# Optimization experiments

Hardware: AMD Instinct MI355X
Metric: run time of the kernel (lower is better)

The kernel has to match this reference:

```python
import jax, jax.numpy as jnp
import numpy as np

D_MODEL = 1024
NUM_HEADS = 16
D_K = D_MODEL // NUM_HEADS


def setup_inputs() -> dict:
    key = jax.random.key(0)
    ks = jax.random.split(key, 5)
    sd = np.sqrt(2.0 / (D_MODEL + D_MODEL))
    x = jax.random.normal(ks[0], (2, 2048, D_MODEL), dtype=jnp.float32)
    # weights stored as [out_features, in_features] like torch Linear
    w_q = jax.random.normal(ks[1], (D_MODEL, D_MODEL), dtype=jnp.float32) * (sd * sd)
    w_k = jax.random.normal(ks[2], (D_MODEL, D_MODEL), dtype=jnp.float32) * (sd * sd)
    w_v = jax.random.normal(ks[3], (D_MODEL, D_MODEL), dtype=jnp.float32) * (sd * sd)
    w_o = jax.random.normal(ks[4], (D_MODEL, D_MODEL), dtype=jnp.float32) * (sd * sd)
    return {"x": x, "w_q": w_q, "w_k": w_k, "w_v": w_v, "w_o": w_o}


def reference(x, w_q, w_k, w_v, w_o):
    B, S, D = x.shape
    H, Dk = NUM_HEADS, D_K
    # projections: x @ W.T
    q = (x @ w_q.T).reshape(B, S, H, Dk).transpose(0, 2, 1, 3)  # [B,H,S,Dk]
    k = (x @ w_k.T).reshape(B, S, H, Dk).transpose(0, 2, 1, 3)
    v = (x @ w_v.T).reshape(B, S, H, Dk).transpose(0, 2, 1, 3)
    scale = 1.0 / np.sqrt(Dk).astype(np.float32)
    scores = jnp.einsum('bhqd,bhkd->bhqk', q, k) * scale  # [B,H,S,S]
    causal = jnp.tril(jnp.ones((S, S), dtype=bool))
    scores = jnp.where(causal, scores, -jnp.inf)
    weights = jax.nn.softmax(scores, axis=-1)
    attn = jnp.einsum('bhqk,bhkd->bhqd', weights, v)  # [B,H,S,Dk]
    attn = attn.transpose(0, 2, 1, 3).reshape(B, S, D)
    return attn @ w_o.T
```

## Files before the change

### kernel.cpp

```cpp
#include <hip/hip_runtime.h>

typedef __attribute__((ext_vector_type(8))) short short8;
typedef __attribute__((ext_vector_type(4))) float f32x4;
typedef __attribute__((ext_vector_type(16))) float f32x16;
typedef __attribute__((ext_vector_type(2))) unsigned int u32x2;

#define DM 1024
#define SL 2048
#define NH 16
#define DKH 64
#define NB 2

__device__ __forceinline__ unsigned short f2bf(float f) {
    union { float f; unsigned int u; } a; a.f = f;
    unsigned int r = a.u + 0x7FFFu + ((a.u >> 16) & 1u);
    return (unsigned short)(r >> 16);
}

__device__ __forceinline__ void gl_lds16(const void* g, void* l) {
    __builtin_amdgcn_global_load_lds(
        (__attribute__((address_space(1))) void*)(g),
        (__attribute__((address_space(3))) void*)(l), 16, 0, 0);
}

__device__ __forceinline__ unsigned int cvtpk_bf16(float lo, float hi) {
    unsigned int r;
    asm("v_cvt_pk_bf16_f32 %0, %1, %2" : "=v"(r) : "v"(lo), "v"(hi));
    return r;
}

__device__ __forceinline__ void pl32swap(unsigned int &a, unsigned int &b) {
    u32x2 r = __builtin_amdgcn_permlane32_swap(a, b, false, false);
    a = r[0]; b = r[1];
}
__device__ __forceinline__ void pl32swapf(float &a, float &b) {
    unsigned int ua = __float_as_uint(a), ub = __float_as_uint(b);
    pl32swap(ua, ub);
    a = __uint_as_float(ua); b = __uint_as_float(ub);
}

__global__ __launch_bounds__(256) void convert_kernel(
    const float* __restrict__ x,  const float* __restrict__ wq,
    const float* __restrict__ wk, const float* __restrict__ wv,
    const float* __restrict__ wo,
    unsigned short* __restrict__ xb,  unsigned short* __restrict__ wqb,
    unsigned short* __restrict__ wkb, unsigned short* __restrict__ wvb,
    unsigned short* __restrict__ wob)
{
    const int NX = NB * SL * DM;
    const int NW = DM * DM;
    int t4 = (blockIdx.x * 256 + threadIdx.x) * 4;
    const float* src; unsigned short* dst; int off; float scale = 1.0f;
    if (t4 < NX)              { src = x;  dst = xb;  off = t4; }
    else if (t4 < NX + NW)    { src = wq; dst = wqb; off = t4 - NX; scale = 0.125f * 1.44269504088896f; }
    else if (t4 < NX + 2*NW)  { src = wk; dst = wkb; off = t4 - NX - NW; }
    else if (t4 < NX + 3*NW)  { src = wv; dst = wvb; off = t4 - NX - 2*NW; }
    else                      { src = wo; dst = wob; off = t4 - NX - 3*NW; }
    float4 v = *(const float4*)(src + off);
    unsigned long long p =
        (unsigned long long)f2bf(v.x * scale)
      | ((unsigned long long)f2bf(v.y * scale) << 16)
      | ((unsigned long long)f2bf(v.z * scale) << 32)
      | ((unsigned long long)f2bf(v.w * scale) << 48);
    *(unsigned long long*)(dst + off) = p;
}

__global__ __launch_bounds__(256) void gemm_bt(
    const unsigned short* __restrict__ A,
    const unsigned short* __restrict__ Bw,
    unsigned short* __restrict__ oq, unsigned short* __restrict__ ok,
    unsigned short* __restrict__ ov)
{
    __shared__ __align__(16) unsigned short As[128 * 64];
    __shared__ __align__(16) unsigned short Bs[128 * 64];
    const int tid  = threadIdx.x;
    const int lane = tid & 63;
    const int wave = tid >> 6;
    const int wm = (wave >> 1) * 64, wn = (wave & 1) * 64;
    const int bx = blockIdx.x, by = blockIdx.y;
    const int c    = lane & 15;
    const int kg16 = (lane >> 4) * 16;
    const int swz  = (c & 7) << 4;

    f32x4 acc[4][4];
    #pragma unroll
    for (int i = 0; i < 4; i++)
        #pragma unroll
        for (int j = 0; j < 4; j++) acc[i][j] = (f32x4){0.f, 0.f, 0.f, 0.f};

    const char* Ab = (const char*)A  + by * 128 * (DM * 2);
    const char* Bb = (const char*)Bw + bx * 128 * (DM * 2);

    for (int k0 = 0; k0 < DM; k0 += 64) {
        #pragma unroll
        for (int i = 0; i < 4; i++) {
            int o  = i * 4096 + tid * 16;
            int r  = o >> 7;
            int cb = o & 127;
            int src = r * (DM * 2) + k0 * 2 + (cb ^ ((r & 7) << 4));
            gl_lds16(Ab + src, (char*)As + o);
            gl_lds16(Bb + src, (char*)Bs + o);
        }
        __syncthreads();
        #pragma unroll
        for (int kk = 0; kk < 2; kk++) {
            short8 a[4], bfr[4];
            #pragma unroll
            for (int mi = 0; mi < 4; mi++)
                a[mi] = *(const short8*)((const char*)As
                        + (wm + mi * 16 + c) * 128 + ((kk * 64 + kg16) ^ swz));
            #pragma unroll
            for (int ni = 0; ni < 4; ni++)
                bfr[ni] = *(const short8*)((const char*)Bs
                        + (wn + ni * 16 + c) * 128 + ((kk * 64 + kg16) ^ swz));
            #pragma unroll
            for (int mi = 0; mi < 4; mi++)
                #pragma unroll
                for (int ni = 0; ni < 4; ni++)
                    acc[mi][ni] = __builtin_amdgcn_mfma_f32_16x16x32_bf16(
                        a[mi], bfr[ni], acc[mi][ni], 0, 0, 0);
        }
        __syncthreads();
    }

    const int r4 = (lane >> 4) * 4;
    const int mat = (bx * 128) >> 10;
    unsigned short* outb = (mat == 0) ? oq : (mat == 1) ? ok : ov;
    const int nb = bx * 128 - (mat << 10);
    #pragma unroll
    for (int mi = 0; mi < 4; mi++) {
        int m_g = by * 128 + wm + mi * 16 + r4;
        int b_  = m_g >> 11, s_ = m_g & 2047;
        #pragma unroll
        for (int ni = 0; ni < 4; ni++) {
            int n_l = nb + wn + ni * 16 + c;
            int h = n_l >> 6, dk = n_l & 63;
            #pragma unroll
            for (int j = 0; j < 4; j++)
                outb[((b_ * NH + h) * SL + (s_ + j)) * DKH + dk] = f2bf(acc[mi][ni][j]);
        }
    }
}

__global__ __launch_bounds__(256) void gemm_o(
    const unsigned short* __restrict__ A,
    const unsigned short* __restrict__ Bw,
    float* __restrict__ of)
{
    __shared__ __align__(16) unsigned short As[64 * 64];
    __shared__ __align__(16) unsigned short Bs[128 * 64];
    const int tid  = threadIdx.x;
    const int lane = tid & 63;
    const int wave = tid >> 6;
    const int wm = (wave >> 1) * 32, wn = (wave & 1) * 64;
    const int bx = blockIdx.x, by = blockIdx.y;
    const int c    = lane & 15;
    const int kg16 = (lane >> 4) * 16;
    const int swz  = (c & 7) << 4;

    f32x4 acc[2][4];
    #pragma unroll
    for (int i = 0; i < 2; i++)
        #pragma unroll
        for (int j = 0; j < 4; j++) acc[i][j] = (f32x4){0.f, 0.f, 0.f, 0.f};

    const char* Ab = (const char*)A  + by * 64  * (DM * 2);
    const char* Bb = (const char*)Bw + bx * 128 * (DM * 2);

    for (int k0 = 0; k0 < DM; k0 += 64) {
        #pragma unroll
        for (int i = 0; i < 2; i++) {
            int o  = i * 4096 + tid * 16;
            int r  = o >> 7, cb = o & 127;
            int src = r * (DM * 2) + k0 * 2 + (cb ^ ((r & 7) << 4));
            gl_lds16(Ab + src, (char*)As + o);
        }
        #pragma unroll
        for (int i = 0; i < 4; i++) {
            int o  = i * 4096 + tid * 16;
            int r  = o >> 7, cb = o & 127;
            int src = r * (DM * 2) + k0 * 2 + (cb ^ ((r & 7) << 4));
            gl_lds16(Bb + src, (char*)Bs + o);
        }
        __syncthreads();
        #pragma unroll
        for (int kk = 0; kk < 2; kk++) {
            short8 a[2], bfr[4];
            #pragma unroll
            for (int mi = 0; mi < 2; mi++)
                a[mi] = *(const short8*)((const char*)As
                        + (wm + mi * 16 + c) * 128 + ((kk * 64 + kg16) ^ swz));
            #pragma unroll
            for (int ni = 0; ni < 4; ni++)
                bfr[ni] = *(const short8*)((const char*)Bs
                        + (wn + ni * 16 + c) * 128 + ((kk * 64 + kg16) ^ swz));
            #pragma unroll
            for (int mi = 0; mi < 2; mi++)
                #pragma unroll
                for (int ni = 0; ni < 4; ni++)
                    acc[mi][ni] = __builtin_amdgcn_mfma_f32_16x16x32_bf16(
                        a[mi], bfr[ni], acc[mi][ni], 0, 0, 0);
        }
        __syncthreads();
    }

    const int r4 = (lane >> 4) * 4;
    #pragma unroll
    for (int mi = 0; mi < 2; mi++) {
        int m_g = by * 64 + wm + mi * 16 + r4;
        #pragma unroll
        for (int ni = 0; ni < 4; ni++) {
            int n_g = bx * 128 + wn + ni * 16 + c;
            #pragma unroll
            for (int j = 0; j < 4; j++)
                of[(m_g + j) * DM + n_g] = acc[mi][ni][j];
        }
    }
}

__global__ __launch_bounds__(128) void attn_kernel(
    const unsigned short* __restrict__ Q,
    const unsigned short* __restrict__ K,
    const unsigned short* __restrict__ V,
    unsigned short* __restrict__ O,
    unsigned short* __restrict__ partO,
    float* __restrict__ ml)
{
    __shared__ __align__(16) unsigned short Kl[2][64 * 64];
    __shared__ __align__(16) unsigned short Vt[2][8 * 64 * 8];
    const int tid = threadIdx.x, lane = tid & 63, wave = tid >> 6;
    const int ln31 = lane & 31, hi = lane >> 5;
    const int item = blockIdx.x >> 5;
    const int bh   = blockIdx.x & 31;
    int qt, cch, t0, ntc;
    if (item < 16)      { qt = 16 + item;              cch = 0; t0 = 0;  ntc = 16; }
    else if (item < 32) { int j = item - 16; qt = 31 - j; cch = 1; t0 = 16; ntc = 16 - j; }
    else                { int j = item - 32; qt = 15 - j; cch = 0; t0 = 0;  ntc = 16 - j; }
    const int b = bh >> 4, h = bh & 15;
    const int bhi = b * NH + h;
    const unsigned short* Qg = Q + bhi * (SL * DKH);
    const unsigned short* Kg = K + bhi * (SL * DKH);
    const unsigned short* Vg = V + bhi * (SL * DKH);
    const int qw = qt * 64 + wave * 32;
    const int vd0 = (tid & 31) * 2, c0 = tid >> 5;
    const int vsw = (vd0 >> 3) & 1;
    const int rsw = (ln31 >> 3) & 1;

    short8 qf[4];
    #pragma unroll
    for (int ks = 0; ks < 4; ks++)
        qf[ks] = *(const short8*)&Qg[(qw + ln31) * DKH + ks * 16 + hi * 8];

    f32x16 OT0, OT1;
    #pragma unroll
    for (int r = 0; r < 16; r++) { OT0[r] = 0.f; OT1[r] = 0.f; }
    float mrun = -1e30f, ls = 0.f;

    unsigned int vreg[16];

    {
        const size_t kvb = (size_t)t0 * 64;
        #pragma unroll
        for (int i = 0; i < 4; i++) {
            int s = i * 128 + tid;
            int kv = s >> 3;
            int k8 = (s & 7) ^ (kv & 7);
            gl_lds16((const char*)Kg + (kvb + kv) * 128 + k8 * 16,
                     (char*)&Kl[0][0] + s * 16);
        }
        #pragma unroll
        for (int c2 = 0; c2 < 2; c2++)
            #pragma unroll
            for (int i = 0; i < 8; i++)
                vreg[c2 * 8 + i] = *(const unsigned int*)&Vg[(kvb + (c0 + 4 * c2) * 8 + i) * DKH + vd0];
    }

    for (int tt = 0; tt < ntc; ++tt) {
        const int t = t0 + tt;
        const int buf = tt & 1;
        const int kv0 = t * 64;
        #pragma unroll
        for (int c2 = 0; c2 < 2; c2++) {
            int chunk = c0 + 4 * c2;
            short8 sa, sb;
            #pragma unroll
            for (int i = 0; i < 8; i++) {
                unsigned int pr = vreg[c2 * 8 + i];
                sa[i] = (short)(pr & 0xFFFFu);
                sb[i] = (short)(pr >> 16);
            }
            int ua = chunk * 64 + vd0;
            *(short8*)&Vt[buf][(ua ^ vsw) * 8]       = sa;
            *(short8*)&Vt[buf][((ua + 1) ^ vsw) * 8] = sb;
        }
        __syncthreads();

        if (tt + 1 < ntc) {
            const size_t kv1 = (size_t)(t + 1) * 64;
            #pragma unroll
            for (int i = 0; i < 4; i++) {
                int s = i * 128 + tid;
                int kv = s >> 3;
                int k8 = (s & 7) ^ (kv & 7);
                gl_lds16((const char*)Kg + (kv1 + kv) * 128 + k8 * 16,
                         (char*)&Kl[buf ^ 1][0] + s * 16);
            }
            #pragma unroll
            for (int c2 = 0; c2 < 2; c2++)
                #pragma unroll
                for (int i = 0; i < 8; i++)
                    vreg[c2 * 8 + i] = *(const unsigned int*)&Vg[(kv1 + (c0 + 4 * c2) * 8 + i) * DKH + vd0];
        }

        const char* kb = (const char*)&Kl[buf][0];
        const unsigned short* vb = &Vt[buf][0];

        f32x16 S0, S1;
        #pragma unroll
        for (int r = 0; r < 16; r++) { S0[r] = 0.f; S1[r] = 0.f; }
        __builtin_amdgcn_s_setprio(1);
        #pragma unroll
        for (int ks = 0; ks < 4; ks++) {
            int ko = (ks * 32 + hi * 16) ^ ((ln31 & 7) << 4);
            short8 ka0 = *(const short8*)(kb + ln31 * 128 + ko);
            short8 ka1 = *(const short8*)(kb + (32 + ln31) * 128 + ko);
            S0 = __builtin_amdgcn_mfma_f32_32x32x16_bf16(ka0, qf[ks], S0, 0, 0, 0);
            S1 = __builtin_amdgcn_mfma_f32_32x32x16_bf16(ka1, qf[ks], S1, 0, 0, 0);
        }
        __builtin_amdgcn_s_setprio(0);

        if (t == qt) {
            const int qrel0 = qw + ln31 - kv0 - 4 * hi;
            const int qrel1 = qrel0 - 32;
            #pragma unroll
            for (int r = 0; r < 16; r++) {
                const int ro = (r & 3) + 8 * (r >> 2);
                if (ro > qrel0) S0[r] = -1e30f;
                if (ro > qrel1) S1[r] = -1e30f;
            }
        }

        float mx = fmaxf(S0[0], S1[0]);
        #pragma unroll
        for (int r = 1; r < 16; r++) mx = fmaxf(mx, fmaxf(S0[r], S1[r]));
        float ma = mx, mb = mx;
        pl32swapf(ma, mb);
        float rm = fmaxf(ma, mb);

        if (__any(rm > mrun + 8.f)) {
            float nm = fmaxf(mrun, rm);
            float corr = __builtin_amdgcn_exp2f(mrun - nm);
            mrun = nm; ls *= corr;
            #pragma unroll
            for (int r = 0; r < 16; r++) { OT0[r] *= corr; OT1[r] *= corr; }
        }

        float psum = 0.f;
        #pragma unroll
        for (int r = 0; r < 16; r++) {
            S0[r] = __builtin_amdgcn_exp2f(S0[r] - mrun); psum += S0[r];
            S1[r] = __builtin_amdgcn_exp2f(S1[r] - mrun); psum += S1[r];
        }
        ls += psum;

        short8 pf[4];
        {
            unsigned int wa, wb, wc, wd;
            wa = cvtpk_bf16(S0[0], S0[1]);   wb = cvtpk_bf16(S0[4], S0[5]);
            pl32swap(wa, wb);
            wc = cvtpk_bf16(S0[2], S0[3]);   wd = cvtpk_bf16(S0[6], S0[7]);
            pl32swap(wc, wd);
            union { unsigned int u[4]; short8 s; } w0 = {{wa, wc, wb, wd}};
            pf[0] = w0.s;

            wa = cvtpk_bf16(S0[8], S0[9]);   wb = cvtpk_bf16(S0[12], S0[13]);
            pl32swap(wa, wb);
            wc = cvtpk_bf16(S0[10], S0[11]); wd = cvtpk_bf16(S0[14], S0[15]);
            pl32swap(wc, wd);
            union { unsigned int u[4]; short8 s; } w1 = {{wa, wc, wb, wd}};
            pf[1] = w1.s;

            wa = cvtpk_bf16(S1[0], S1[1]);   wb = cvtpk_bf16(S1[4], S1[5]);
            pl32swap(wa, wb);
            wc = cvtpk_bf16(S1[2], S1[3]);   wd = cvtpk_bf16(S1[6], S1[7]);
            pl32swap(wc, wd);
            union { unsigned int u[4]; short8 s; } w2 = {{wa, wc, wb, wd}};
            pf[2] = w2.s;

            wa = cvtpk_bf16(S1[8], S1[9]);   wb = cvtpk_bf16(S1[12], S1[13]);
            pl32swap(wa, wb);
            wc = cvtpk_bf16(S1[10], S1[11]); wd = cvtpk_bf16(S1[14], S1[15]);
            pl32swap(wc, wd);
            union { unsigned int u[4]; short8 s; } w3 = {{wa, wc, wb, wd}};
            pf[3] = w3.s;
        }

        __builtin_amdgcn_s_setprio(1);
        #pragma unroll
        for (int ks2 = 0; ks2 < 4; ks2++) {
            int slot = (ks2 * 2 + hi) * 64;
            int r0u = slot + ln31;
            int r1u = slot + 32 + ln31;
            short8 va0 = *(const short8*)&vb[(r0u ^ rsw) * 8];
            short8 va1 = *(const short8*)&vb[(r1u ^ rsw) * 8];
            OT0 = __builtin_amdgcn_mfma_f32_32x32x16_bf16(va0, pf[ks2], OT0, 0, 0, 0);
            OT1 = __builtin_amdgcn_mfma_f32_32x32x16_bf16(va1, pf[ks2], OT1, 0, 0, 0);
        }
        __builtin_amdgcn_s_setprio(0);
    }

    float la = ls, lb = ls;
    pl32swapf(la, lb);
    const float lrow = la + lb;
    const int qrow_l = wave * 32 + ln31;
    if (qt >= 16) {
        const int rec = (bh * 16 + (qt - 16)) * 2 + cch;
        unsigned short* po = partO + (size_t)rec * 4096;
        if (hi == 0) {
            ml[(rec * 64 + qrow_l) * 2]     = mrun;
            ml[(rec * 64 + qrow_l) * 2 + 1] = lrow;
        }
        #pragma unroll
        for (int r = 0; r < 16; r++) {
            const int d0 = (r & 3) + 8 * (r >> 2) + 4 * hi;
            po[qrow_l * 64 + d0]      = f2bf(OT0[r]);
            po[qrow_l * 64 + 32 + d0] = f2bf(OT1[r]);
        }
    } else {
        float inv = 1.0f / lrow;
        const int qrow = qw + ln31;
        const size_t base = (size_t)(b * SL + qrow) * DM + h * DKH;
        #pragma unroll
        for (int r = 0; r < 16; r++) {
            const int d0 = (r & 3) + 8 * (r >> 2) + 4 * hi;
            O[base + d0]      = f2bf(OT0[r] * inv);
            O[base + 32 + d0] = f2bf(OT1[r] * inv);
        }
    }
}

__global__ __launch_bounds__(256) void combine_kernel(
    const unsigned short* __restrict__ partO,
    const float* __restrict__ ml,
    unsigned short* __restrict__ O)
{
    const int gi = blockIdx.x * 8 + (threadIdx.x >> 5);
    const int ln = threadIdx.x & 31;
    const int bh = gi >> 10, rem = gi & 1023;
    const int qtl = rem >> 6, row = rem & 63;
    const int qt = 16 + qtl;
    const int rec0 = (bh * 16 + qtl) * 2;
    const float m0 = ml[(rec0 * 64 + row) * 2];
    const float l0 = ml[(rec0 * 64 + row) * 2 + 1];
    const float m1 = ml[((rec0 + 1) * 64 + row) * 2];
    const float l1 = ml[((rec0 + 1) * 64 + row) * 2 + 1];
    const float M  = fmaxf(m0, m1);
    const float w0 = exp2f(m0 - M), w1 = exp2f(m1 - M);
    const float inv = 1.0f / (w0 * l0 + w1 * l1);
    const unsigned int u0 = *(const unsigned int*)&partO[(size_t)rec0 * 4096 + row * 64 + ln * 2];
    const unsigned int u1 = *(const unsigned int*)&partO[(size_t)(rec0 + 1) * 4096 + row * 64 + ln * 2];
    const float a0 = __uint_as_float(u0 << 16);
    const float b0 = __uint_as_float(u0 & 0xFFFF0000u);
    const float a1 = __uint_as_float(u1 << 16);
    const float b1 = __uint_as_float(u1 & 0xFFFF0000u);
    const float oa = (a0 * w0 + a1 * w1) * inv;
    const float ob = (b0 * w0 + b1 * w1) * inv;
    const unsigned int pack = (unsigned int)f2bf(oa) | ((unsigned int)f2bf(ob) << 16);
    const int b = bh >> 4, h = bh & 15;
    const size_t base = (size_t)(b * SL + qt * 64 + row) * DM + h * DKH;
    *(unsigned int*)&O[base + ln * 2] = pack;
}

extern "C" void kernel_launch(void* const* d_in, const int* in_sizes, int n_in,
                              void* d_out, int out_size, void* d_ws, size_t ws_size,
                              hipStream_t stream)
{
    const float* x  = (const float*)d_in[0];
    const float* wq = (const float*)d_in[1];
    const float* wk = (const float*)d_in[2];
    const float* wv = (const float*)d_in[3];
    const float* wo = (const float*)d_in[4];
    char* ws = (char*)d_ws;
    unsigned short* xb  = (unsigned short*)(ws);
    unsigned short* wqb = (unsigned short*)(ws + (8ll  << 20));
    unsigned short* wkb = (unsigned short*)(ws + (10ll << 20));
    unsigned short* wvb = (unsigned short*)(ws + (12ll << 20));
    unsigned short* wob = (unsigned short*)(ws + (14ll << 20));
    unsigned short* Qb  = (unsigned short*)(ws + (16ll << 20));
    unsigned short* Kb  = (unsigned short*)(ws + (24ll << 20));
    unsigned short* Vb  = (unsigned short*)(ws + (32ll << 20));
    unsigned short* Abf = (unsigned short*)(ws + (40ll << 20));
    unsigned short* partO = (unsigned short*)(ws);
    float*          mlbuf = (float*)(ws + (8ll << 20));
    float* out = (float*)d_out;

    convert_kernel<<<dim3(8192), dim3(256), 0, stream>>>(
        x, wq, wk, wv, wo, xb, wqb, wkb, wvb, wob);

    gemm_bt<<<dim3(24, 32), dim3(256), 0, stream>>>(xb, wqb, Qb, Kb, Vb);

    attn_kernel<<<dim3(1536), dim3(128), 0, stream>>>(Qb, Kb, Vb, Abf, partO, mlbuf);
    combine_kernel<<<dim3(4096), dim3(256), 0, stream>>>(partO, mlbuf, Abf);

    gemm_o<<<dim3(8, 64), dim3(256), 0, stream>>>(Abf, wob, out);
}
```

Measured before the change: 104.9 us.

## Fuse split-KV combine into output projection GEMM A-tile loading

Removes the separate combine kernel and instead merges the two partial attention outputs (with their max/sum statistics) while loading A tiles inside gemm_o for the later query tiles. This drops a kernel launch and a round-trip write/read of the combined attention buffer. In exchange, the fused blocks do synchronous vector loads plus exp/divide math in the GEMM main loop instead of async global-to-LDS copies, and each combine is recomputed by every one of the 8 column blocks.

```diff
diff --git a/kernel.cpp b/kernel.cpp
--- a/kernel.cpp
+++ b/kernel.cpp
@@ -4,6 +4,7 @@
 typedef __attribute__((ext_vector_type(4))) float f32x4;
 typedef __attribute__((ext_vector_type(16))) float f32x16;
 typedef __attribute__((ext_vector_type(2))) unsigned int u32x2;
+typedef __attribute__((ext_vector_type(4))) unsigned int u32x4;
 
 #define DM 1024
 #define SL 2048
@@ -144,6 +145,8 @@
 
 __global__ __launch_bounds__(256) void gemm_o(
     const unsigned short* __restrict__ A,
+    const unsigned short* __restrict__ partO,
+    const float* __restrict__ ml,
     const unsigned short* __restrict__ Bw,
     float* __restrict__ of)
 {
@@ -158,6 +161,13 @@
     const int kg16 = (lane >> 4) * 16;
     const int swz  = (c & 7) << 4;
 
+    const int m0g  = by * 64;
+    const int s_   = m0g & 2047;
+    const int qt   = s_ >> 6;
+    const int bb   = m0g >> 11;
+    const bool fuse = (qt >= 16);
+    const int qtl  = qt - 16;
+
     f32x4 acc[2][4];
     #pragma unroll
     for (int i = 0; i < 2; i++)
@@ -168,12 +178,49 @@
     const char* Bb = (const char*)Bw + bx * 128 * (DM * 2);
 
     for (int k0 = 0; k0 < DM; k0 += 64) {
-        #pragma unroll
-        for (int i = 0; i < 2; i++) {
-            int o  = i * 4096 + tid * 16;
-            int r  = o >> 7, cb = o & 127;
-            int src = r * (DM * 2) + k0 * 2 + (cb ^ ((r & 7) << 4));
-            gl_lds16(Ab + src, (char*)As + o);
+        if (!fuse) {
+            #pragma unroll
+            for (int i = 0; i < 2; i++) {
+                int o  = i * 4096 + tid * 16;
+                int r  = o >> 7, cb = o & 127;
+                int src = r * (DM * 2) + k0 * 2 + (cb ^ ((r & 7) << 4));
+                gl_lds16(Ab + src, (char*)As + o);
+            }
+        } else {
+            const int h = k0 >> 6;
+            const int rec0 = ((bb * 16 + h) * 16 + qtl) * 2;
+            const char* p0 = (const char*)partO + (size_t)rec0 * 8192;
+            const char* p1 = p0 + 8192;
+            #pragma unroll
+            for (int i = 0; i < 2; i++) {
+                int o  = i * 4096 + tid * 16;
+                int r  = o >> 7, cb = o & 127;
+                int sco = r * 128 + (cb ^ ((r & 7) << 4));
+                float m0v = ml[(rec0 * 64 + r) * 2];
+                float l0v = ml[(rec0 * 64 + r) * 2 + 1];
+                float m1v = ml[((rec0 + 1) * 64 + r) * 2];
+                float l1v = ml[((rec0 + 1) * 64 + r) * 2 + 1];
+                float M   = fmaxf(m0v, m1v);
+                float w0  = __builtin_amdgcn_exp2f(m0v - M);
+                float w1  = __builtin_amdgcn_exp2f(m1v - M);
+                float inv = 1.0f / (w0 * l0v + w1 * l1v);
+                float fw0 = w0 * inv, fw1 = w1 * inv;
+                u32x4 u0 = *(const u32x4*)(p0 + sco);
+                u32x4 u1 = *(const u32x4*)(p1 + sco);
+                u32x4 ow;
+                #pragma unroll
+                for (int q = 0; q < 4; q++) {
+                    unsigned int a0 = u0[q], a1 = u1[q];
+                    float alo = __uint_as_float(a0 << 16);
+                    float ahi = __uint_as_float(a0 & 0xFFFF0000u);
+                    float clo = __uint_as_float(a1 << 16);
+                    float chi = __uint_as_float(a1 & 0xFFFF0000u);
+                    float rlo = alo * fw0 + clo * fw1;
+                    float rhi = ahi * fw0 + chi * fw1;
+                    ow[q] = cvtpk_bf16(rlo, rhi);
+                }
+                *(u32x4*)((char*)As + o) = ow;
+            }
         }
         #pragma unroll
         for (int i = 0; i < 4; i++) {
@@ -439,38 +486,6 @@
     }
 }
 
-__global__ __launch_bounds__(256) void combine_kernel(
-    const unsigned short* __restrict__ partO,
-    const float* __restrict__ ml,
-    unsigned short* __restrict__ O)
-{
-    const int gi = blockIdx.x * 8 + (threadIdx.x >> 5);
-    const int ln = threadIdx.x & 31;
-    const int bh = gi >> 10, rem = gi & 1023;
-    const int qtl = rem >> 6, row = rem & 63;
-    const int qt = 16 + qtl;
-    const int rec0 = (bh * 16 + qtl) * 2;
-    const float m0 = ml[(rec0 * 64 + row) * 2];
-    const float l0 = ml[(rec0 * 64 + row) * 2 + 1];
-    const float m1 = ml[((rec0 + 1) * 64 + row) * 2];
-    const float l1 = ml[((rec0 + 1) * 64 + row) * 2 + 1];
-    const float M  = fmaxf(m0, m1);
-    const float w0 = exp2f(m0 - M), w1 = exp2f(m1 - M);
-    const float inv = 1.0f / (w0 * l0 + w1 * l1);
-    const unsigned int u0 = *(const unsigned int*)&partO[(size_t)rec0 * 4096 + row * 64 + ln * 2];
-    const unsigned int u1 = *(const unsigned int*)&partO[(size_t)(rec0 + 1) * 4096 + row * 64 + ln * 2];
-    const float a0 = __uint_as_float(u0 << 16);
-    const float b0 = __uint_as_float(u0 & 0xFFFF0000u);
-    const float a1 = __uint_as_float(u1 << 16);
-    const float b1 = __uint_as_float(u1 & 0xFFFF0000u);
-    const float oa = (a0 * w0 + a1 * w1) * inv;
-    const float ob = (b0 * w0 + b1 * w1) * inv;
-    const unsigned int pack = (unsigned int)f2bf(oa) | ((unsigned int)f2bf(ob) << 16);
-    const int b = bh >> 4, h = bh & 15;
-    const size_t base = (size_t)(b * SL + qt * 64 + row) * DM + h * DKH;
-    *(unsigned int*)&O[base + ln * 2] = pack;
-}
-
 extern "C" void kernel_launch(void* const* d_in, const int* in_sizes, int n_in,
                               void* d_out, int out_size, void* d_ws, size_t ws_size,
                               hipStream_t stream)
@@ -500,7 +515,6 @@
     gemm_bt<<<dim3(24, 32), dim3(256), 0, stream>>>(xb, wqb, Qb, Kb, Vb);
 
     attn_kernel<<<dim3(1536), dim3(128), 0, stream>>>(Qb, Kb, Vb, Abf, partO, mlbuf);
-    combine_kernel<<<dim3(4096), dim3(256), 0, stream>>>(partO, mlbuf, Abf);
-
-    gemm_o<<<dim3(8, 64), dim3(256), 0, stream>>>(Abf, wob, out);
-}
+
+    gemm_o<<<dim3(8, 64), dim3(256), 0, stream>>>(Abf, partO, mlbuf, wob, out);
+}
```

Result: slower. 113.5 us (+8.2%).
